# Kernel tuning notes

Measured on AMD Instinct MI355X. Metric: run time of the kernel, lower is better.

## Reference

```python
import jax, jax.numpy as jnp
import numpy as np

NEG_SLOPE = 0.2


def gat_conv(x, src, dst, W, a_src, a_dst, bias, concat, num_nodes):
    # x: [N, F_in]; W: [F_in, H*C]; a_src/a_dst: [H, C]
    H, C = a_src.shape
    h = (x @ W).reshape(num_nodes, H, C)               # [N,H,C]
    alpha_s = jnp.sum(h * a_src[None], axis=-1)        # [N,H]
    alpha_d = jnp.sum(h * a_dst[None], axis=-1)        # [N,H]
    e = jax.nn.leaky_relu(alpha_s[src] + alpha_d[dst], NEG_SLOPE)  # [E,H]
    m = jax.ops.segment_max(e, dst, num_segments=num_nodes)
    m = jnp.where(jnp.isfinite(m), m, 0.0)
    ex = jnp.exp(e - m[dst])
    denom = jax.ops.segment_sum(ex, dst, num_segments=num_nodes)
    alpha = ex / (denom[dst] + 1e-16)                  # scatter-softmax over dst
    msg = h[src] * alpha[:, :, None]                   # [E,H,C]
    out = jax.ops.segment_sum(msg, dst, num_segments=num_nodes)  # [N,H,C]
    if concat:
        out = out.reshape(num_nodes, H * C)
    else:
        out = out.mean(axis=1)
    return out + bias


def setup_inputs() -> dict:
    key = jax.random.key(0)
    ks = jax.random.split(key, 12)
    N, E = 50000, 800000
    num_concat, F_in, hid, H1, H2, n_cls = 2, 128, 64, 4, 1, 16
    x_list = jax.random.normal(ks[0], (num_concat, N, F_in), dtype=jnp.float32)
    edge_index = jax.random.randint(ks[1], (2, E), 0, N, dtype=jnp.int64)
    s = 0.1
    W1 = jax.random.normal(ks[2], (num_concat, F_in, H1 * hid), dtype=jnp.float32) * s
    att_src1 = jax.random.normal(ks[3], (num_concat, H1, hid), dtype=jnp.float32) * s
    att_dst1 = jax.random.normal(ks[4], (num_concat, H1, hid), dtype=jnp.float32) * s
    bias1 = jnp.zeros((num_concat, H1 * hid), dtype=jnp.float32)
    W2 = jax.random.normal(ks[5], (hid * H1 * num_concat, H2 * n_cls), dtype=jnp.float32) * s
    att_src2 = jax.random.normal(ks[6], (H2, n_cls), dtype=jnp.float32) * s
    att_dst2 = jax.random.normal(ks[7], (H2, n_cls), dtype=jnp.float32) * s
    bias2 = jnp.zeros((n_cls,), dtype=jnp.float32)
    return {"x_list": x_list, "edge_index": edge_index,
            "W1": W1, "att_src1": att_src1, "att_dst1": att_dst1, "bias1": bias1,
            "W2": W2, "att_src2": att_src2, "att_dst2": att_dst2, "bias2": bias2}


def reference(x_list, edge_index, W1, att_src1, att_dst1, bias1, W2, att_src2, att_dst2, bias2):
    num_concat, N, _ = x_list.shape
    loop = jnp.arange(N, dtype=edge_index.dtype)
    src = jnp.concatenate([edge_index[0], loop])  # PyG add_self_loops=True
    dst = jnp.concatenate([edge_index[1], loop])
    hidden = [jax.nn.elu(gat_conv(x_list[k], src, dst, W1[k], att_src1[k], att_dst1[k],
                                  bias1[k], True, N))
              for k in range(num_concat)]
    x = jnp.concatenate(hidden, axis=-1)           # [N, hid*H1*num_concat]
    out = gat_conv(x, src, dst, W2, att_src2, att_dst2, bias2, False, N)
    return out
```

## Files before the change

### kernel.cpp

```cpp
#include <hip/hip_runtime.h>

#define LEAKY(v) ((v) >= 0.0f ? (v) : 0.2f * (v))

typedef __attribute__((ext_vector_type(8))) short bf16x8;
typedef __attribute__((ext_vector_type(4))) float f32x4;

__device__ __forceinline__ unsigned short f2bf(float f) {
    unsigned int u = __float_as_uint(f);
    unsigned int r = u + 0x7FFFu + ((u >> 16) & 1u);
    return (unsigned short)(r >> 16);
}
__device__ __forceinline__ unsigned int pk2(float a, float b) {
    return (unsigned int)f2bf(a) | ((unsigned int)f2bf(b) << 16);
}
__device__ __forceinline__ float lo16(unsigned int u) { return __uint_as_float(u << 16); }
__device__ __forceinline__ float hi16(unsigned int u) { return __uint_as_float(u & 0xFFFF0000u); }


__global__ __launch_bounds__(256) void count_deg(const int* ei, int* deg, int E, int Etot) {
    int i = blockIdx.x * 256 + threadIdx.x;
    if (i >= Etot) return;
    int d = (i < E) ? ei[E + i] : (i - E);
    atomicAdd(&deg[d], 1);
}

__global__ __launch_bounds__(512) void scan_block(const int* deg, int* excl, int* bsum, int n) {
    __shared__ int s[512];
    int t = threadIdx.x;
    int i = blockIdx.x * 512 + t;
    int v = (i < n) ? deg[i] : 0;
    s[t] = v;
    __syncthreads();
    for (int d = 1; d < 512; d <<= 1) {
        int x = 0;
        if (t >= d) x = s[t - d];
        __syncthreads();
        if (t >= d) s[t] += x;
        __syncthreads();
    }
    if (i < n) excl[i] = s[t] - v;
    if (t == 511) bsum[blockIdx.x] = s[511];
}

__global__ __launch_bounds__(512) void scan_sums(const int* bsum, int* boff, int nb) {
    __shared__ int s[512];
    int t = threadIdx.x;
    int v = (t < nb) ? bsum[t] : 0;
    s[t] = v;
    __syncthreads();
    for (int d = 1; d < 512; d <<= 1) {
        int x = 0;
        if (t >= d) x = s[t - d];
        __syncthreads();
        if (t >= d) s[t] += x;
        __syncthreads();
    }
    boff[t] = s[t] - v;
}

__global__ __launch_bounds__(256) void finalize_off(int* csr, int* cursor, const int* boff, int n, int etot) {
    int i = blockIdx.x * 256 + threadIdx.x;
    if (i < n) {
        int v = csr[i] + boff[i >> 9];
        csr[i] = v;
        cursor[i] = v;
    }
    if (i == 0) csr[n] = etot;
}

__global__ __launch_bounds__(256) void scatter_edge(const int* ei, int* cursor, int* srcs, int* dsts,
                                                    int E, int Etot) {
    int i = blockIdx.x * 256 + threadIdx.x;
    if (i >= Etot) return;
    int s, d;
    if (i < E) { s = ei[i]; d = ei[E + i]; }
    else       { s = i - E; d = s; }
    int pos = atomicAdd(&cursor[d], 1);
    srcs[pos] = s;
    dsts[pos] = d;
}


__global__ __launch_bounds__(256) void wpack1(const float* __restrict__ W1, unsigned short* __restrict__ wt1) {
    int id = blockIdx.x * 256 + threadIdx.x;
    if (id >= 8192) return;
    int conv = id >> 12, rem = id & 4095;
    int c = rem >> 4, q = rem & 15;
    const float* src = W1 + (size_t)conv * 32768 + (size_t)(q * 8) * 256 + c;
    float w[8];
#pragma unroll
    for (int j = 0; j < 8; ++j) w[j] = src[j * 256];
    uint4 v;
    v.x = pk2(w[0], w[1]); v.y = pk2(w[2], w[3]);
    v.z = pk2(w[4], w[5]); v.w = pk2(w[6], w[7]);
    *(uint4*)(wt1 + (size_t)conv * 32768 + c * 128 + ((q ^ (c & 7)) << 3)) = v;
}

__global__ __launch_bounds__(256) void wpack2(const float* __restrict__ W2, unsigned short* __restrict__ wt2) {
    int id = blockIdx.x * 256 + threadIdx.x;
    if (id >= 1024) return;
    int s = id >> 6, l = id & 63;
    const float* src = W2 + (size_t)(s * 32 + (l >> 4) * 8) * 16 + (l & 15);
    float w[8];
#pragma unroll
    for (int j = 0; j < 8; ++j) w[j] = src[j * 16];
    uint4 v;
    v.x = pk2(w[0], w[1]); v.y = pk2(w[2], w[3]);
    v.z = pk2(w[4], w[5]); v.w = pk2(w[6], w[7]);
    *(uint4*)(wt2 + (size_t)id * 8) = v;
}


__global__ __launch_bounds__(256) void gemm1_mfma(const float* __restrict__ x_list,
                                                  const unsigned short* __restrict__ wt1,
                                                  const float* __restrict__ asw, const float* __restrict__ adw,
                                                  unsigned short* __restrict__ hp,
                                                  float* __restrict__ as1, float* __restrict__ ad1, int N) {
    __shared__ unsigned short As[64 * 128];
    __shared__ unsigned short Ws[256 * 128];
    int conv = blockIdx.y;
    int t = threadIdx.x;
    int w = t >> 6, l = t & 63;

    const float* xg = x_list + (size_t)conv * N * 128;
#pragma unroll
    for (int p = 0; p < 4; ++p) {
        int id = p * 256 + t;
        int row = id >> 4, q = id & 15;
        int grow = blockIdx.x * 64 + row;
        uint4 v = make_uint4(0, 0, 0, 0);
        if (grow < N) {
            const float* src = xg + (size_t)grow * 128 + q * 8;
            float4 a = *(const float4*)src;
            float4 b = *(const float4*)(src + 4);
            v.x = pk2(a.x, a.y); v.y = pk2(a.z, a.w);
            v.z = pk2(b.x, b.y); v.w = pk2(b.z, b.w);
        }
        *(uint4*)(As + row * 128 + ((q ^ (row & 7)) << 3)) = v;
    }
    const uint4* wsrc = (const uint4*)(wt1 + (size_t)conv * 32768);
#pragma unroll
    for (int p = 0; p < 16; ++p) {
        int id = p * 256 + t;
        *(uint4*)(Ws + (size_t)id * 8) = wsrc[id];
    }
    __syncthreads();

    f32x4 acc[4][4];
#pragma unroll
    for (int mt = 0; mt < 4; ++mt)
#pragma unroll
        for (int nt = 0; nt < 4; ++nt) acc[mt][nt] = (f32x4){0.f, 0.f, 0.f, 0.f};

    int lr = l & 15, lg = l >> 4;
#pragma unroll
    for (int s = 0; s < 4; ++s) {
        int kq = s * 4 + lg;
        bf16x8 af[4], bf[4];
#pragma unroll
        for (int mt = 0; mt < 4; ++mt) {
            int r = mt * 16 + lr;
            af[mt] = *(const bf16x8*)(As + r * 128 + ((kq ^ (r & 7)) << 3));
        }
#pragma unroll
        for (int nt = 0; nt < 4; ++nt) {
            int c = w * 64 + nt * 16 + lr;
            bf[nt] = *(const bf16x8*)(Ws + c * 128 + ((kq ^ (c & 7)) << 3));
        }
#pragma unroll
        for (int mt = 0; mt < 4; ++mt)
#pragma unroll
            for (int nt = 0; nt < 4; ++nt)
                acc[mt][nt] = __builtin_amdgcn_mfma_f32_16x16x32_bf16(af[mt], bf[nt], acc[mt][nt], 0, 0, 0);
    }

    float aswv[4], adwv[4];
#pragma unroll
    for (int nt = 0; nt < 4; ++nt) {
        aswv[nt] = asw[conv * 256 + w * 64 + nt * 16 + lr];
        adwv[nt] = adw[conv * 256 + w * 64 + nt * 16 + lr];
    }
#pragma unroll
    for (int mt = 0; mt < 4; ++mt) {
#pragma unroll
        for (int i = 0; i < 4; ++i) {
            int grow = blockIdx.x * 64 + mt * 16 + lg * 4 + i;
            bool ok = grow < N;
            float sv = 0.f, dv = 0.f;
#pragma unroll
            for (int nt = 0; nt < 4; ++nt) {
                float hv = acc[mt][nt][i];
                if (ok) hp[(size_t)grow * 512 + (nt * 16 + lr) * 8 + conv * 4 + w] = f2bf(hv);
                sv += hv * aswv[nt];
                dv += hv * adwv[nt];
            }
#pragma unroll
            for (int o = 1; o < 16; o <<= 1) {
                sv += __shfl_xor(sv, o);
                dv += __shfl_xor(dv, o);
            }
            if (lr == 0 && ok) {
                as1[((size_t)conv * N + grow) * 4 + w] = sv;
                ad1[((size_t)conv * N + grow) * 4 + w] = dv;
            }
        }
    }
}


__global__ __launch_bounds__(256) void edge_w1(const int* __restrict__ srcs, const int* __restrict__ dsts,
                                               const float* __restrict__ as, const float* __restrict__ ad,
                                               float* __restrict__ pw, int Etot, int N4) {
    int e = blockIdx.x * 256 + threadIdx.x;
    if (e >= Etot) return;
    int s = srcs[e], d = dsts[e];
    float4 a0 = *(const float4*)(as + (size_t)s * 4);
    float4 b0 = *(const float4*)(ad + (size_t)d * 4);
    float4 a1 = *(const float4*)(as + N4 + (size_t)s * 4);
    float4 b1 = *(const float4*)(ad + N4 + (size_t)d * 4);
    float4 p0, p1;
    p0.x = __expf(LEAKY(a0.x + b0.x));
    p0.y = __expf(LEAKY(a0.y + b0.y));
    p0.z = __expf(LEAKY(a0.z + b0.z));
    p0.w = __expf(LEAKY(a0.w + b0.w));
    p1.x = __expf(LEAKY(a1.x + b1.x));
    p1.y = __expf(LEAKY(a1.y + b1.y));
    p1.z = __expf(LEAKY(a1.z + b1.z));
    p1.w = __expf(LEAKY(a1.w + b1.w));
    *(float4*)(pw + (size_t)e * 8)     = p0;
    *(float4*)(pw + (size_t)e * 8 + 4) = p1;
}


#define ACC8(g, pa, pb) {                                                      \
    den[0] += (pa).x; acc[0] += (pa).x * lo16((g).x);                          \
    den[1] += (pa).y; acc[1] += (pa).y * hi16((g).x);                          \
    den[2] += (pa).z; acc[2] += (pa).z * lo16((g).y);                          \
    den[3] += (pa).w; acc[3] += (pa).w * hi16((g).y);                          \
    den[4] += (pb).x; acc[4] += (pb).x * lo16((g).z);                          \
    den[5] += (pb).y; acc[5] += (pb).y * hi16((g).z);                          \
    den[6] += (pb).z; acc[6] += (pb).z * lo16((g).w);                          \
    den[7] += (pb).w; acc[7] += (pb).w * hi16((g).w); }

__global__ __launch_bounds__(256) void agg1_both(const unsigned short* __restrict__ hp,
                                                 const float* __restrict__ pw,
                                                 const int* __restrict__ off, const int* __restrict__ srcs,
                                                 const float* __restrict__ b1,
                                                 unsigned short* __restrict__ x2, int N) {
    int n = blockIdx.x * 4 + (threadIdx.x >> 6);
    int lane = threadIdx.x & 63;
    if (n >= N) return;
    int r0 = off[n], r1 = off[n + 1];

    float acc[8] = {0.f, 0.f, 0.f, 0.f, 0.f, 0.f, 0.f, 0.f};
    float den[8] = {0.f, 0.f, 0.f, 0.f, 0.f, 0.f, 0.f, 0.f};

    for (int base = r0; base < r1; base += 64) {
        int cnt = min(64, r1 - base);
        int my = (base + lane < r1) ? srcs[base + lane] : 0;
        int j = 0;
        for (; j + 2 <= cnt; j += 2) {
            int s0 = __shfl(my, j);
            int s1 = __shfl(my, j + 1);
            uint4 g0 = *(const uint4*)(hp + (size_t)s0 * 512 + lane * 8);
            uint4 g1 = *(const uint4*)(hp + (size_t)s1 * 512 + lane * 8);
            float4 pa0 = *(const float4*)(pw + (size_t)(base + j) * 8);
            float4 pb0 = *(const float4*)(pw + (size_t)(base + j) * 8 + 4);
            float4 pa1 = *(const float4*)(pw + (size_t)(base + j + 1) * 8);
            float4 pb1 = *(const float4*)(pw + (size_t)(base + j + 1) * 8 + 4);
            ACC8(g0, pa0, pb0);
            ACC8(g1, pa1, pb1);
        }
        if (j < cnt) {
            int s0 = __shfl(my, j);
            uint4 g0 = *(const uint4*)(hp + (size_t)s0 * 512 + lane * 8);
            float4 pa0 = *(const float4*)(pw + (size_t)(base + j) * 8);
            float4 pb0 = *(const float4*)(pw + (size_t)(base + j) * 8 + 4);
            ACC8(g0, pa0, pb0);
        }
    }

    unsigned short* xo = x2 + (size_t)n * 512;
#pragma unroll
    for (int q = 0; q < 8; ++q) {
        int k = q >> 2, hd = q & 3;
        int ofs = k * 256 + hd * 64 + lane;
        float o = acc[q] / (den[q] + 1e-16f) + b1[ofs];
        o = o > 0.f ? o : (__expf(o) - 1.0f);
        xo[ofs] = f2bf(o);
    }
}


__global__ __launch_bounds__(256) void gemm2_mfma(const unsigned short* __restrict__ x2,
                                                  const unsigned short* __restrict__ wt2,
                                                  const float* __restrict__ asw2, const float* __restrict__ adw2,
                                                  float* __restrict__ h2,
                                                  float* __restrict__ as2, float* __restrict__ ad2, int N) {
    int t = threadIdx.x;
    int w = t >> 6, l = t & 63;
    int rowbase = (blockIdx.x * 4 + w) * 16;
    if (rowbase >= N) return;
    int lr = l & 15, lg = l >> 4;

    f32x4 acc = (f32x4){0.f, 0.f, 0.f, 0.f};
    const unsigned short* ap = x2 + (size_t)(rowbase + lr) * 512 + lg * 8;
#pragma unroll
    for (int s = 0; s < 16; ++s) {
        bf16x8 av = *(const bf16x8*)(ap + s * 32);
        bf16x8 bv = *(const bf16x8*)(wt2 + ((size_t)s * 64 + l) * 8);
        acc = __builtin_amdgcn_mfma_f32_16x16x32_bf16(av, bv, acc, 0, 0, 0);
    }

    float asv = asw2[lr], adv = adw2[lr];
#pragma unroll
    for (int i = 0; i < 4; ++i) {
        int row = rowbase + lg * 4 + i;
        if (row < N) h2[(size_t)row * 16 + lr] = acc[i];
        float sv = acc[i] * asv, dv = acc[i] * adv;
#pragma unroll
        for (int o = 1; o < 16; o <<= 1) {
            sv += __shfl_xor(sv, o);
            dv += __shfl_xor(dv, o);
        }
        if (lr == 0 && row < N) { as2[row] = sv; ad2[row] = dv; }
    }
}


__global__ __launch_bounds__(256) void agg2(const float* __restrict__ h2,
                                            const float* __restrict__ as2, const float* __restrict__ ad2,
                                            const int* __restrict__ off, const int* __restrict__ srcs,
                                            const float* __restrict__ bias2, float* __restrict__ out, int N) {
    int n = blockIdx.x * 4 + (threadIdx.x >> 6);
    int lane = threadIdx.x & 63;
    if (n >= N) return;
    int r0 = off[n], r1 = off[n + 1];
    float adn = ad2[n];
    int cg = lane & 3, eo = lane >> 2;

    float4 acc = make_float4(0.f, 0.f, 0.f, 0.f);
    float den = 0.f;
    for (int base = r0; base + eo < r1; base += 16) {
        int e = base + eo;
        int s = srcs[e];
        float p = __expf(LEAKY(as2[s] + adn));
        float4 hv = *(const float4*)(h2 + (size_t)s * 16 + cg * 4);
        den += p;
        acc.x += p * hv.x; acc.y += p * hv.y;
        acc.z += p * hv.z; acc.w += p * hv.w;
    }
#pragma unroll
    for (int o = 4; o < 64; o <<= 1) {
        acc.x += __shfl_xor(acc.x, o);
        acc.y += __shfl_xor(acc.y, o);
        acc.z += __shfl_xor(acc.z, o);
        acc.w += __shfl_xor(acc.w, o);
        den   += __shfl_xor(den, o);
    }
    if (eo == 0) {
        float inv = 1.f / (den + 1e-16f);
        float4 b = *(const float4*)(bias2 + cg * 4);
        float4 o4;
        o4.x = acc.x * inv + b.x;
        o4.y = acc.y * inv + b.y;
        o4.z = acc.z * inv + b.z;
        o4.w = acc.w * inv + b.w;
        *(float4*)(out + (size_t)n * 16 + cg * 4) = o4;
    }
}


extern "C" void kernel_launch(void* const* d_in, const int* in_sizes, int n_in,
                              void* d_out, int out_size, void* d_ws, size_t ws_size,
                              hipStream_t stream) {
    const float* x_list = (const float*)d_in[0];
    const int*   ei     = (const int*)d_in[1];
    const float* W1     = (const float*)d_in[2];
    const float* as1w   = (const float*)d_in[3];
    const float* ad1w   = (const float*)d_in[4];
    const float* b1     = (const float*)d_in[5];
    const float* W2     = (const float*)d_in[6];
    const float* as2w   = (const float*)d_in[7];
    const float* ad2w   = (const float*)d_in[8];
    const float* b2     = (const float*)d_in[9];
    float* out = (float*)d_out;

    const int N = in_sizes[0] / 256;
    const int E = in_sizes[1] / 2;
    const int Etot = E + N;
    const int N4 = N * 4;

    char* ws = (char*)d_ws;
    size_t woff = 0;
    auto alloc = [&](size_t bytes) {
        char* p = ws + woff;
        woff = (woff + bytes + 255) & ~(size_t)255;
        return p;
    };
    int*   csr    = (int*)alloc((size_t)(N + 1) * 4);
    int*   cursor = (int*)alloc((size_t)N * 4);
    int*   srcs   = (int*)alloc((size_t)Etot * 4);
    int*   dsts   = (int*)alloc((size_t)Etot * 4);
    int*   bsum   = (int*)alloc(512 * 4);
    int*   boff   = (int*)alloc(512 * 4);
    float* as1    = (float*)alloc((size_t)N4 * 2 * 4);
    float* ad1    = (float*)alloc((size_t)N4 * 2 * 4);
    float* as2    = (float*)alloc((size_t)N * 4);
    float* ad2    = (float*)alloc((size_t)N * 4);
    unsigned short* wt1 = (unsigned short*)alloc(2 * 32768 * 2);
    unsigned short* wt2 = (unsigned short*)alloc(16 * 64 * 8 * 2);
    unsigned short* hp  = (unsigned short*)alloc((size_t)N * 512 * 2);
    unsigned short* x2  = (unsigned short*)alloc((size_t)N * 512 * 2);
    float* h2     = (float*)alloc((size_t)N * 16 * 4);
    float* pw     = (float*)alloc((size_t)Etot * 8 * 4);

    hipMemsetAsync(cursor, 0, (size_t)N * 4, stream);
    int gE = (Etot + 255) / 256;
    count_deg<<<gE, 256, 0, stream>>>(ei, cursor, E, Etot);
    int nb = (N + 511) / 512;
    scan_block<<<nb, 512, 0, stream>>>(cursor, csr, bsum, N);
    scan_sums<<<1, 512, 0, stream>>>(bsum, boff, nb);
    finalize_off<<<(N + 255) / 256, 256, 0, stream>>>(csr, cursor, boff, N, Etot);
    scatter_edge<<<gE, 256, 0, stream>>>(ei, cursor, srcs, dsts, E, Etot);

    wpack1<<<32, 256, 0, stream>>>(W1, wt1);
    wpack2<<<4, 256, 0, stream>>>(W2, wt2);

    gemm1_mfma<<<dim3((N + 63) / 64, 2), 256, 0, stream>>>(x_list, wt1, as1w, ad1w, hp, as1, ad1, N);
    edge_w1<<<gE, 256, 0, stream>>>(srcs, dsts, as1, ad1, pw, Etot, N4);
    agg1_both<<<(N + 3) / 4, 256, 0, stream>>>(hp, pw, csr, srcs, b1, x2, N);

    gemm2_mfma<<<(N + 63) / 64, 256, 0, stream>>>(x2, wt2, as2w, ad2w, h2, as2, ad2, N);
    agg2<<<(N + 3) / 4, 256, 0, stream>>>(h2, as2, ad2, csr, srcs, b2, out, N);
}
```

Before: 328.4 us.

## Fuse edge attention weights into aggregation and change hidden layout to contiguous heads

Removes the separate edge_w1 kernel and its per-edge weight buffer. Each lane of agg1 now computes the exponentiated leaky-relu score on the fly from a packed per-node [src|dst] attention array. The dst edge array is also dropped. gemm1 swaps the MFMA operand order so each lane holds contiguous output columns, which lets it write hp in head-contiguous order with packed stores, and agg1 writes x2 with one 16-byte store per lane. The trade is redundant exp computation per lane (eight lanes per head) in exchange for less global memory traffic and one fewer launch.

Measured after the change: 311.9 us. 5.0% less time.

```diff
diff --git a/kernel.cpp b/kernel.cpp
--- a/kernel.cpp
+++ b/kernel.cpp
@@ -68,8 +68,7 @@
     if (i == 0) csr[n] = etot;
 }
 
-__global__ __launch_bounds__(256) void scatter_edge(const int* ei, int* cursor, int* srcs, int* dsts,
-                                                    int E, int Etot) {
+__global__ __launch_bounds__(256) void scatter_src(const int* ei, int* cursor, int* srcs, int E, int Etot) {
     int i = blockIdx.x * 256 + threadIdx.x;
     if (i >= Etot) return;
     int s, d;
@@ -77,7 +76,6 @@
     else       { s = i - E; d = s; }
     int pos = atomicAdd(&cursor[d], 1);
     srcs[pos] = s;
-    dsts[pos] = d;
 }
 
 
@@ -115,7 +113,7 @@
                                                   const unsigned short* __restrict__ wt1,
                                                   const float* __restrict__ asw, const float* __restrict__ adw,
                                                   unsigned short* __restrict__ hp,
-                                                  float* __restrict__ as1, float* __restrict__ ad1, int N) {
+                                                  float* __restrict__ aad, int N) {
     __shared__ unsigned short As[64 * 128];
     __shared__ unsigned short Ws[256 * 128];
     int conv = blockIdx.y;
@@ -171,79 +169,44 @@
         for (int mt = 0; mt < 4; ++mt)
 #pragma unroll
             for (int nt = 0; nt < 4; ++nt)
-                acc[mt][nt] = __builtin_amdgcn_mfma_f32_16x16x32_bf16(af[mt], bf[nt], acc[mt][nt], 0, 0, 0);
-    }
-
-    float aswv[4], adwv[4];
+                acc[mt][nt] = __builtin_amdgcn_mfma_f32_16x16x32_bf16(bf[nt], af[mt], acc[mt][nt], 0, 0, 0);
+    }
+
+    float4 aswv[4], adwv[4];
 #pragma unroll
     for (int nt = 0; nt < 4; ++nt) {
-        aswv[nt] = asw[conv * 256 + w * 64 + nt * 16 + lr];
-        adwv[nt] = adw[conv * 256 + w * 64 + nt * 16 + lr];
+        aswv[nt] = *(const float4*)(asw + conv * 256 + w * 64 + nt * 16 + lg * 4);
+        adwv[nt] = *(const float4*)(adw + conv * 256 + w * 64 + nt * 16 + lg * 4);
     }
 #pragma unroll
     for (int mt = 0; mt < 4; ++mt) {
-#pragma unroll
-        for (int i = 0; i < 4; ++i) {
-            int grow = blockIdx.x * 64 + mt * 16 + lg * 4 + i;
-            bool ok = grow < N;
-            float sv = 0.f, dv = 0.f;
-#pragma unroll
-            for (int nt = 0; nt < 4; ++nt) {
-                float hv = acc[mt][nt][i];
-                if (ok) hp[(size_t)grow * 512 + (nt * 16 + lr) * 8 + conv * 4 + w] = f2bf(hv);
-                sv += hv * aswv[nt];
-                dv += hv * adwv[nt];
+        int grow = blockIdx.x * 64 + mt * 16 + lr;
+        bool ok = grow < N;
+        float sv = 0.f, dv = 0.f;
+#pragma unroll
+        for (int nt = 0; nt < 4; ++nt) {
+            f32x4 a = acc[mt][nt];
+            if (ok) {
+                uint2 pk;
+                pk.x = pk2(a[0], a[1]);
+                pk.y = pk2(a[2], a[3]);
+                *(uint2*)(hp + (size_t)grow * 512 + conv * 256 + w * 64 + nt * 16 + lg * 4) = pk;
             }
-#pragma unroll
-            for (int o = 1; o < 16; o <<= 1) {
-                sv += __shfl_xor(sv, o);
-                dv += __shfl_xor(dv, o);
-            }
-            if (lr == 0 && ok) {
-                as1[((size_t)conv * N + grow) * 4 + w] = sv;
-                ad1[((size_t)conv * N + grow) * 4 + w] = dv;
-            }
-        }
-    }
-}
-
-
-__global__ __launch_bounds__(256) void edge_w1(const int* __restrict__ srcs, const int* __restrict__ dsts,
-                                               const float* __restrict__ as, const float* __restrict__ ad,
-                                               float* __restrict__ pw, int Etot, int N4) {
-    int e = blockIdx.x * 256 + threadIdx.x;
-    if (e >= Etot) return;
-    int s = srcs[e], d = dsts[e];
-    float4 a0 = *(const float4*)(as + (size_t)s * 4);
-    float4 b0 = *(const float4*)(ad + (size_t)d * 4);
-    float4 a1 = *(const float4*)(as + N4 + (size_t)s * 4);
-    float4 b1 = *(const float4*)(ad + N4 + (size_t)d * 4);
-    float4 p0, p1;
-    p0.x = __expf(LEAKY(a0.x + b0.x));
-    p0.y = __expf(LEAKY(a0.y + b0.y));
-    p0.z = __expf(LEAKY(a0.z + b0.z));
-    p0.w = __expf(LEAKY(a0.w + b0.w));
-    p1.x = __expf(LEAKY(a1.x + b1.x));
-    p1.y = __expf(LEAKY(a1.y + b1.y));
-    p1.z = __expf(LEAKY(a1.z + b1.z));
-    p1.w = __expf(LEAKY(a1.w + b1.w));
-    *(float4*)(pw + (size_t)e * 8)     = p0;
-    *(float4*)(pw + (size_t)e * 8 + 4) = p1;
-}
-
-
-#define ACC8(g, pa, pb) {                                                      \
-    den[0] += (pa).x; acc[0] += (pa).x * lo16((g).x);                          \
-    den[1] += (pa).y; acc[1] += (pa).y * hi16((g).x);                          \
-    den[2] += (pa).z; acc[2] += (pa).z * lo16((g).y);                          \
-    den[3] += (pa).w; acc[3] += (pa).w * hi16((g).y);                          \
-    den[4] += (pb).x; acc[4] += (pb).x * lo16((g).z);                          \
-    den[5] += (pb).y; acc[5] += (pb).y * hi16((g).z);                          \
-    den[6] += (pb).z; acc[6] += (pb).z * lo16((g).w);                          \
-    den[7] += (pb).w; acc[7] += (pb).w * hi16((g).w); }
+            sv += a[0] * aswv[nt].x + a[1] * aswv[nt].y + a[2] * aswv[nt].z + a[3] * aswv[nt].w;
+            dv += a[0] * adwv[nt].x + a[1] * adwv[nt].y + a[2] * adwv[nt].z + a[3] * adwv[nt].w;
+        }
+        sv += __shfl_xor(sv, 16); sv += __shfl_xor(sv, 32);
+        dv += __shfl_xor(dv, 16); dv += __shfl_xor(dv, 32);
+        if (l < 16 && ok) {
+            aad[(size_t)grow * 16 + conv * 4 + w]     = sv;
+            aad[(size_t)grow * 16 + 8 + conv * 4 + w] = dv;
+        }
+    }
+}
+
 
 __global__ __launch_bounds__(256) void agg1_both(const unsigned short* __restrict__ hp,
-                                                 const float* __restrict__ pw,
+                                                 const float* __restrict__ aad,
                                                  const int* __restrict__ off, const int* __restrict__ srcs,
                                                  const float* __restrict__ b1,
                                                  unsigned short* __restrict__ x2, int N) {
@@ -251,9 +214,11 @@
     int lane = threadIdx.x & 63;
     if (n >= N) return;
     int r0 = off[n], r1 = off[n + 1];
+    int ch = lane >> 3;
+    float ad_l = aad[(size_t)n * 16 + 8 + ch];
 
     float acc[8] = {0.f, 0.f, 0.f, 0.f, 0.f, 0.f, 0.f, 0.f};
-    float den[8] = {0.f, 0.f, 0.f, 0.f, 0.f, 0.f, 0.f, 0.f};
+    float den = 0.f;
 
     for (int base = r0; base < r1; base += 64) {
         int cnt = min(64, r1 - base);
@@ -264,31 +229,46 @@
             int s1 = __shfl(my, j + 1);
             uint4 g0 = *(const uint4*)(hp + (size_t)s0 * 512 + lane * 8);
             uint4 g1 = *(const uint4*)(hp + (size_t)s1 * 512 + lane * 8);
-            float4 pa0 = *(const float4*)(pw + (size_t)(base + j) * 8);
-            float4 pb0 = *(const float4*)(pw + (size_t)(base + j) * 8 + 4);
-            float4 pa1 = *(const float4*)(pw + (size_t)(base + j + 1) * 8);
-            float4 pb1 = *(const float4*)(pw + (size_t)(base + j + 1) * 8 + 4);
-            ACC8(g0, pa0, pb0);
-            ACC8(g1, pa1, pb1);
+            float a0 = aad[(size_t)s0 * 16 + ch];
+            float a1 = aad[(size_t)s1 * 16 + ch];
+            float p0 = __expf(LEAKY(a0 + ad_l));
+            float p1 = __expf(LEAKY(a1 + ad_l));
+            den += p0; den += p1;
+            acc[0] += p0 * lo16(g0.x); acc[1] += p0 * hi16(g0.x);
+            acc[2] += p0 * lo16(g0.y); acc[3] += p0 * hi16(g0.y);
+            acc[4] += p0 * lo16(g0.z); acc[5] += p0 * hi16(g0.z);
+            acc[6] += p0 * lo16(g0.w); acc[7] += p0 * hi16(g0.w);
+            acc[0] += p1 * lo16(g1.x); acc[1] += p1 * hi16(g1.x);
+            acc[2] += p1 * lo16(g1.y); acc[3] += p1 * hi16(g1.y);
+            acc[4] += p1 * lo16(g1.z); acc[5] += p1 * hi16(g1.z);
+            acc[6] += p1 * lo16(g1.w); acc[7] += p1 * hi16(g1.w);
         }
         if (j < cnt) {
             int s0 = __shfl(my, j);
             uint4 g0 = *(const uint4*)(hp + (size_t)s0 * 512 + lane * 8);
-            float4 pa0 = *(const float4*)(pw + (size_t)(base + j) * 8);
-            float4 pb0 = *(const float4*)(pw + (size_t)(base + j) * 8 + 4);
-            ACC8(g0, pa0, pb0);
-        }
-    }
-
-    unsigned short* xo = x2 + (size_t)n * 512;
-#pragma unroll
-    for (int q = 0; q < 8; ++q) {
-        int k = q >> 2, hd = q & 3;
-        int ofs = k * 256 + hd * 64 + lane;
-        float o = acc[q] / (den[q] + 1e-16f) + b1[ofs];
-        o = o > 0.f ? o : (__expf(o) - 1.0f);
-        xo[ofs] = f2bf(o);
-    }
+            float a0 = aad[(size_t)s0 * 16 + ch];
+            float p0 = __expf(LEAKY(a0 + ad_l));
+            den += p0;
+            acc[0] += p0 * lo16(g0.x); acc[1] += p0 * hi16(g0.x);
+            acc[2] += p0 * lo16(g0.y); acc[3] += p0 * hi16(g0.y);
+            acc[4] += p0 * lo16(g0.z); acc[5] += p0 * hi16(g0.z);
+            acc[6] += p0 * lo16(g0.w); acc[7] += p0 * hi16(g0.w);
+        }
+    }
+
+    float inv = 1.f / (den + 1e-16f);
+    const float* bp = b1 + lane * 8;
+    unsigned int ow[4];
+#pragma unroll
+    for (int q = 0; q < 4; ++q) {
+        float o0 = acc[q * 2 + 0] * inv + bp[q * 2 + 0];
+        float o1 = acc[q * 2 + 1] * inv + bp[q * 2 + 1];
+        o0 = o0 > 0.f ? o0 : (__expf(o0) - 1.0f);
+        o1 = o1 > 0.f ? o1 : (__expf(o1) - 1.0f);
+        ow[q] = pk2(o0, o1);
+    }
+    uint4 ov = make_uint4(ow[0], ow[1], ow[2], ow[3]);
+    *(uint4*)(x2 + (size_t)n * 512 + lane * 8) = ov;
 }
 
 
@@ -389,7 +369,6 @@
     const int N = in_sizes[0] / 256;
     const int E = in_sizes[1] / 2;
     const int Etot = E + N;
-    const int N4 = N * 4;
 
     char* ws = (char*)d_ws;
     size_t woff = 0;
@@ -401,11 +380,9 @@
     int*   csr    = (int*)alloc((size_t)(N + 1) * 4);
     int*   cursor = (int*)alloc((size_t)N * 4);
     int*   srcs   = (int*)alloc((size_t)Etot * 4);
-    int*   dsts   = (int*)alloc((size_t)Etot * 4);
     int*   bsum   = (int*)alloc(512 * 4);
     int*   boff   = (int*)alloc(512 * 4);
-    float* as1    = (float*)alloc((size_t)N4 * 2 * 4);
-    float* ad1    = (float*)alloc((size_t)N4 * 2 * 4);
+    float* aad    = (float*)alloc((size_t)N * 16 * 4);
     float* as2    = (float*)alloc((size_t)N * 4);
     float* ad2    = (float*)alloc((size_t)N * 4);
     unsigned short* wt1 = (unsigned short*)alloc(2 * 32768 * 2);
@@ -413,7 +390,6 @@
     unsigned short* hp  = (unsigned short*)alloc((size_t)N * 512 * 2);
     unsigned short* x2  = (unsigned short*)alloc((size_t)N * 512 * 2);
     float* h2     = (float*)alloc((size_t)N * 16 * 4);
-    float* pw     = (float*)alloc((size_t)Etot * 8 * 4);
 
     hipMemsetAsync(cursor, 0, (size_t)N * 4, stream);
     int gE = (Etot + 255) / 256;
@@ -422,14 +398,13 @@
     scan_block<<<nb, 512, 0, stream>>>(cursor, csr, bsum, N);
     scan_sums<<<1, 512, 0, stream>>>(bsum, boff, nb);
     finalize_off<<<(N + 255) / 256, 256, 0, stream>>>(csr, cursor, boff, N, Etot);
-    scatter_edge<<<gE, 256, 0, stream>>>(ei, cursor, srcs, dsts, E, Etot);
+    scatter_src<<<gE, 256, 0, stream>>>(ei, cursor, srcs, E, Etot);
 
     wpack1<<<32, 256, 0, stream>>>(W1, wt1);
     wpack2<<<4, 256, 0, stream>>>(W2, wt2);
 
-    gemm1_mfma<<<dim3((N + 63) / 64, 2), 256, 0, stream>>>(x_list, wt1, as1w, ad1w, hp, as1, ad1, N);
-    edge_w1<<<gE, 256, 0, stream>>>(srcs, dsts, as1, ad1, pw, Etot, N4);
-    agg1_both<<<(N + 3) / 4, 256, 0, stream>>>(hp, pw, csr, srcs, b1, x2, N);
+    gemm1_mfma<<<dim3((N + 63) / 64, 2), 256, 0, stream>>>(x_list, wt1, as1w, ad1w, hp, aad, N);
+    agg1_both<<<(N + 3) / 4, 256, 0, stream>>>(hp, aad, csr, srcs, b1, x2, N);
 
     gemm2_mfma<<<(N + 63) / 64, 256, 0, stream>>>(x2, wt2, as2w, ad2w, h2, as2, ad2, N);
     agg2<<<(N + 3) / 4, 256, 0, stream>>>(h2, as2, ad2, csr, srcs, b2, out, N);
```
